# Kernel optimization log

Measured on AMD Instinct MI355X. Metric: run time of the kernel, lower is better.

## Reference

```python
import jax, jax.numpy as jnp
import numpy as np

N_EMBD = 1024
N_HEAD = 16
B, T = 2, 2048
LN_EPS = 1e-5


def _linear_params(key, d_in, d_out):
    k1, k2 = jax.random.split(key)
    bound = 1.0 / np.sqrt(d_in)
    W = jax.random.uniform(k1, (d_in, d_out), jnp.float32, -bound, bound)
    b = jax.random.uniform(k2, (d_out,), jnp.float32, -bound, bound)
    return W, b


def setup_inputs() -> dict:
    key = jax.random.key(0)
    ks = jax.random.split(key, 8)
    x = jax.random.normal(ks[0], (B, T, N_EMBD), jnp.float32)
    Wq, bq = _linear_params(ks[1], N_EMBD, N_EMBD)
    Wk, bk = _linear_params(ks[2], N_EMBD, N_EMBD)
    Wv, bv = _linear_params(ks[3], N_EMBD, N_EMBD)
    Wo, bo = _linear_params(ks[4], N_EMBD, N_EMBD)
    W1, b1 = _linear_params(ks[5], N_EMBD, 4 * N_EMBD)
    W2, b2 = _linear_params(ks[6], 4 * N_EMBD, N_EMBD)
    ln1_g = jnp.ones((N_EMBD,), jnp.float32)
    ln1_b = jnp.zeros((N_EMBD,), jnp.float32)
    ln2_g = jnp.ones((N_EMBD,), jnp.float32)
    ln2_b = jnp.zeros((N_EMBD,), jnp.float32)
    return dict(x=x, Wq=Wq, bq=bq, Wk=Wk, bk=bk, Wv=Wv, bv=bv, Wo=Wo, bo=bo,
                W1=W1, b1=b1, W2=W2, b2=b2,
                ln1_g=ln1_g, ln1_b=ln1_b, ln2_g=ln2_g, ln2_b=ln2_b)


def _layernorm(x, g, b):
    mu = jnp.mean(x, axis=-1, keepdims=True)
    var = jnp.mean(jnp.square(x - mu), axis=-1, keepdims=True)
    return (x - mu) * jax.lax.rsqrt(var + LN_EPS) * g + b


def _attention(x, Wq, bq, Wk, bk, Wv, bv, Wo, bo):
    Bsz, Tlen, C = x.shape
    hd = C // N_HEAD
    q = (x @ Wq + bq).reshape(Bsz, Tlen, N_HEAD, hd)
    k = (x @ Wk + bk).reshape(Bsz, Tlen, N_HEAD, hd)
    v = (x @ Wv + bv).reshape(Bsz, Tlen, N_HEAD, hd)
    scale = 1.0 / np.sqrt(hd)
    # NOTE: the original module's mask buffer is all ones -> masked_fill is a
    # no-op, so attention is FULL (non-causal) despite the class name.
    att = jnp.einsum('bqhd,bkhd->bhqk', q, k) * scale
    att = jax.nn.softmax(att, axis=-1)
    y = jnp.einsum('bhqk,bkhd->bqhd', att, v).reshape(Bsz, Tlen, C)
    return y @ Wo + bo


def reference(x, Wq, bq, Wk, bk, Wv, bv, Wo, bo, W1, b1, W2, b2,
              ln1_g, ln1_b, ln2_g, ln2_b):
    x = x + _attention(_layernorm(x, ln1_g, ln1_b), Wq, bq, Wk, bk, Wv, bv, Wo, bo)
    h = _layernorm(x, ln2_g, ln2_b)
    h = jax.nn.gelu(h @ W1 + b1, approximate=False) @ W2 + b2
    return x + h
```

## Files before the change

### kernel.cpp

```cpp
#include <hip/hip_runtime.h>
#include <hip/hip_bf16.h>
#include <math.h>


typedef __bf16 bf16x8 __attribute__((ext_vector_type(8)));
typedef float f32x4 __attribute__((ext_vector_type(4)));

__device__ __forceinline__ unsigned short f2bf(float f) {
  union { float f; unsigned int u; } v; v.f = f;
  unsigned int u = v.u;
  unsigned int r = (u + 0x7fffu + ((u >> 16) & 1u)) >> 16;
  return (unsigned short)r;
}

__device__ __forceinline__ unsigned int fbits(float f) {
  union { float f; unsigned int u; } v; v.f = f;
  return v.u;
}

__device__ __forceinline__ bf16x8 ld_bf16x8(const unsigned short* p) {
  union { uint4 u; bf16x8 v; } x;
  x.u = *(const uint4*)p;
  return x.v;
}

__device__ __forceinline__ float fast_exp2(float x) {
#if __has_builtin(__builtin_amdgcn_exp2f)
  return __builtin_amdgcn_exp2f(x);
#else
  return exp2f(x);
#endif
}

__device__ __forceinline__ void async_copy16(const void* g, void* l) {
  __builtin_amdgcn_global_load_lds(
      (const __attribute__((address_space(1))) void*)g,
      (__attribute__((address_space(3))) void*)l, 16, 0, 0);
}

__global__ __launch_bounds__(256) void transpose_cast_kernel(
    const float* __restrict__ W, unsigned short* __restrict__ Wt, int N, int K) {
  __shared__ unsigned short tile[32][33];
  const int n0 = blockIdx.x * 32, k0 = blockIdx.y * 32;
  const int t = threadIdx.x;
  const int r = t >> 3, cq = (t & 7) * 4;
  float4 v = *(const float4*)&W[(size_t)(k0 + r) * N + n0 + cq];
  tile[cq + 0][r] = f2bf(v.x);
  tile[cq + 1][r] = f2bf(v.y);
  tile[cq + 2][r] = f2bf(v.z);
  tile[cq + 3][r] = f2bf(v.w);
  __syncthreads();
  ushort4 o;
  o.x = tile[r][cq + 0];
  o.y = tile[r][cq + 1];
  o.z = tile[r][cq + 2];
  o.w = tile[r][cq + 3];
  *(ushort4*)&Wt[(size_t)(n0 + r) * K + k0 + cq] = o;
}

__global__ __launch_bounds__(256) void transpose_v_kernel(
    const unsigned short* __restrict__ V, unsigned short* __restrict__ Vt) {
  __shared__ unsigned short tile[32][36];
  const int kt = blockIdx.x * 32;
  const int d0 = blockIdx.y * 32;
  const int bh = blockIdx.z;
  const int bb = bh >> 4, h = bh & 15;
  const int t = threadIdx.x;
  const int r = t >> 3, c4 = (t & 7) * 4;
  ushort4 v = *(const ushort4*)&V[((size_t)bb * 2048 + kt + r) * 1024 + h * 64 + d0 + c4];
  tile[c4 + 0][r] = v.x;
  tile[c4 + 1][r] = v.y;
  tile[c4 + 2][r] = v.z;
  tile[c4 + 3][r] = v.w;
  __syncthreads();
  ushort4 o;
  o.x = tile[r][c4 + 0];
  o.y = tile[r][c4 + 1];
  o.z = tile[r][c4 + 2];
  o.w = tile[r][c4 + 3];
  *(ushort4*)&Vt[((size_t)bh * 64 + d0 + r) * 2048 + kt + c4] = o;
}

__global__ __launch_bounds__(256) void ln_kernel(
    const float* __restrict__ x, const float* __restrict__ g,
    const float* __restrict__ b, unsigned short* __restrict__ out) {
  const int row = blockIdx.x, t = threadIdx.x;
  const float4 v = ((const float4*)(x + (size_t)row * 1024))[t];
  float s = v.x + v.y + v.z + v.w;
  float s2 = v.x * v.x + v.y * v.y + v.z * v.z + v.w * v.w;
  for (int o = 32; o > 0; o >>= 1) {
    s += __shfl_xor(s, o, 64);
    s2 += __shfl_xor(s2, o, 64);
  }
  __shared__ float red[8];
  const int w = t >> 6;
  if ((t & 63) == 0) { red[w] = s; red[4 + w] = s2; }
  __syncthreads();
  s = red[0] + red[1] + red[2] + red[3];
  s2 = red[4] + red[5] + red[6] + red[7];
  const float mu = s * (1.f / 1024.f);
  const float var = s2 * (1.f / 1024.f) - mu * mu;
  const float rs = rsqrtf(var + 1e-5f);
  const float4 gg = ((const float4*)g)[t];
  const float4 bb = ((const float4*)b)[t];
  ushort4 o4;
  o4.x = f2bf((v.x - mu) * rs * gg.x + bb.x);
  o4.y = f2bf((v.y - mu) * rs * gg.y + bb.y);
  o4.z = f2bf((v.z - mu) * rs * gg.z + bb.z);
  o4.w = f2bf((v.w - mu) * rs * gg.w + bb.w);
  ((ushort4*)(out + (size_t)row * 1024))[t] = o4;
}

enum { MODE_QKV = 0, MODE_RES = 1, MODE_GELU = 2 };

#define QSCALE 0.18033688011112043f

template <int BM, int BN, int MODE>
__global__ __launch_bounds__(256) void gemm_kernel(
    const unsigned short* __restrict__ A, const unsigned short* __restrict__ Bt,
    const float* __restrict__ bias0, const float* __restrict__ bias1,
    const float* __restrict__ bias2, const float* __restrict__ residual,
    void* __restrict__ out0, void* __restrict__ out1, void* __restrict__ out2,
    int M, int N, int K) {
  constexpr int MI = BM / 32;
  constexpr int NI = BN / 32;
  __shared__ __align__(16) unsigned short As[2][2][BM * 32];
  __shared__ __align__(16) unsigned short Bs[2][2][BN * 32];
  const int t = threadIdx.x;

  const int NT = N / BN;
  const int NTX = NT >> 3;
  const int bid = blockIdx.x;
  const int xcd = bid & 7, local = bid >> 3;
  const int nt_ = xcd * NTX + local % NTX;
  const int mt = local / NTX;
  const int m0 = mt * BM, n0 = nt_ * BN;

  const int l = t & 63, w = t >> 6;
  const int wm = (w >> 1) * (BM / 2), wn = (w & 1) * (BN / 2);
  const int lr = l & 15, lq = l >> 4;

  f32x4 acc[MI][NI];
#pragma unroll
  for (int i = 0; i < MI; i++)
#pragma unroll
    for (int j = 0; j < NI; j++) {
      f32x4 z = {0.f, 0.f, 0.f, 0.f};
      acc[i][j] = z;
    }

  auto issue = [&](int k0, int p) {
#pragma unroll
    for (int h = 0; h < 2; h++)
#pragma unroll
      for (int s = 0; s < BM / 64; s++) {
        const int c = t + s * 256;
        const int row = c >> 2, k8 = (c & 3) * 8;
        async_copy16(&A[(size_t)(m0 + row) * K + k0 + h * 32 + k8],
                     &As[p][h][c * 8]);
      }
#pragma unroll
    for (int h = 0; h < 2; h++)
#pragma unroll
      for (int s = 0; s < BN / 64; s++) {
        const int c = t + s * 256;
        const int row = c >> 2, k8 = (c & 3) * 8;
        async_copy16(&Bt[(size_t)(n0 + row) * K + k0 + h * 32 + k8],
                     &Bs[p][h][c * 8]);
      }
  };

  issue(0, 0);
  int p = 0;
  for (int k0 = 0; k0 < K; k0 += 64) {
    __syncthreads();
    if (k0 + 64 < K) issue(k0 + 64, p ^ 1);
#pragma unroll
    for (int kk = 0; kk < 2; kk++) {
      bf16x8 af[MI], bf[NI];
#pragma unroll
      for (int mi = 0; mi < MI; mi++)
        af[mi] = ld_bf16x8(&As[p][kk][(wm + mi * 16 + lr) * 32 + lq * 8]);
#pragma unroll
      for (int ni = 0; ni < NI; ni++)
        bf[ni] = ld_bf16x8(&Bs[p][kk][(wn + ni * 16 + lr) * 32 + lq * 8]);
#pragma unroll
      for (int mi = 0; mi < MI; mi++)
#pragma unroll
        for (int ni = 0; ni < NI; ni++)
          acc[mi][ni] = __builtin_amdgcn_mfma_f32_16x16x32_bf16(
              af[mi], bf[ni], acc[mi][ni], 0, 0, 0);
    }
    p ^= 1;
  }

#pragma unroll
  for (int mi = 0; mi < MI; mi++) {
#pragma unroll
    for (int ni = 0; ni < NI; ni++) {
#pragma unroll
      for (int i = 0; i < 4; i++) {
        const int gm = m0 + wm + mi * 16 + lq * 4 + i;
        const int gn = n0 + wn + ni * 16 + lr;
        const float v = acc[mi][ni][i];
        if (MODE == MODE_QKV) {
          const int sel = gn >> 10, cn = gn & 1023;
          const float* bb = sel == 0 ? bias0 : (sel == 1 ? bias1 : bias2);
          unsigned short* dst =
              (unsigned short*)(sel == 0 ? out0 : (sel == 1 ? out1 : out2));
          float u = v + bb[cn];
          if (sel == 0) u *= QSCALE;
          dst[(size_t)gm * 1024 + cn] = f2bf(u);
        } else if (MODE == MODE_RES) {
          ((float*)out0)[(size_t)gm * N + gn] =
              v + bias0[gn] + residual[(size_t)gm * N + gn];
        } else {
          const float u = v + bias0[gn];
          const float ge = 0.5f * u * (1.f + erff(u * 0.70710678118654752f));
          ((unsigned short*)out0)[(size_t)gm * N + gn] = f2bf(ge);
        }
      }
    }
  }
}

__global__ __launch_bounds__(256) void attn_kernel(
    const unsigned short* __restrict__ Q, const unsigned short* __restrict__ Kt,
    const unsigned short* __restrict__ Vt, unsigned short* __restrict__ O) {
  __shared__ __align__(16) unsigned short Ps[128 * 72];
  const int id = blockIdx.x;
  const int xcd = id & 7, loc = id >> 3;
  const int bh = xcd * 4 + (loc >> 4);
  const int qt = loc & 15;
  const int bb = bh >> 4, h = bh & 15;
  const int t = threadIdx.x, l = t & 63, w = t >> 6;
  const int lr = l & 15, lq = l >> 4;
  const size_t rowBase = (size_t)bb * 2048;
  const int col0 = h * 64;

  bf16x8 qf[2][2];
#pragma unroll
  for (int s = 0; s < 2; s++)
#pragma unroll
    for (int kk = 0; kk < 2; kk++)
      qf[s][kk] = ld_bf16x8(
          &Q[(rowBase + qt * 128 + w * 32 + s * 16 + lr) * 1024 + col0 +
             kk * 32 + lq * 8]);

  bf16x8 kf[2][4];
#pragma unroll
  for (int nt = 0; nt < 4; nt++)
#pragma unroll
    for (int kk = 0; kk < 2; kk++)
      kf[kk][nt] = ld_bf16x8(
          &Kt[(rowBase + nt * 16 + lr) * 1024 + col0 + kk * 32 + lq * 8]);

  f32x4 oacc[2][4];
#pragma unroll
  for (int s = 0; s < 2; s++)
#pragma unroll
    for (int nt = 0; nt < 4; nt++) {
      f32x4 z = {0.f, 0.f, 0.f, 0.f};
      oacc[s][nt] = z;
    }
  float lp[2] = {0.f, 0.f};

  for (int kt = 0; kt < 2048; kt += 64) {
    bf16x8 vf[2][4];
#pragma unroll
    for (int nt = 0; nt < 4; nt++)
#pragma unroll
      for (int kb = 0; kb < 2; kb++)
        vf[kb][nt] = ld_bf16x8(
            &Vt[((size_t)bh * 64 + nt * 16 + lr) * 2048 + kt + kb * 32 +
                lq * 8]);

    f32x4 st[2][4];
#pragma unroll
    for (int s = 0; s < 2; s++)
#pragma unroll
      for (int nt = 0; nt < 4; nt++) {
        f32x4 z = {0.f, 0.f, 0.f, 0.f};
        st[s][nt] = z;
      }
#pragma unroll
    for (int nt = 0; nt < 4; nt++) {
      __builtin_amdgcn_s_setprio(1);
      st[0][nt] = __builtin_amdgcn_mfma_f32_16x16x32_bf16(kf[0][nt], qf[0][0], st[0][nt], 0, 0, 0);
      st[1][nt] = __builtin_amdgcn_mfma_f32_16x16x32_bf16(kf[0][nt], qf[1][0], st[1][nt], 0, 0, 0);
      st[0][nt] = __builtin_amdgcn_mfma_f32_16x16x32_bf16(kf[1][nt], qf[0][1], st[0][nt], 0, 0, 0);
      st[1][nt] = __builtin_amdgcn_mfma_f32_16x16x32_bf16(kf[1][nt], qf[1][1], st[1][nt], 0, 0, 0);
      __builtin_amdgcn_s_setprio(0);
    }

    const int ktn = (kt + 64) & 2047;
#pragma unroll
    for (int nt = 0; nt < 4; nt++)
#pragma unroll
      for (int kk = 0; kk < 2; kk++)
        kf[kk][nt] = ld_bf16x8(
            &Kt[(rowBase + ktn + nt * 16 + lr) * 1024 + col0 + kk * 32 +
                lq * 8]);

#pragma unroll
    for (int s = 0; s < 2; s++) {
      float rsum = 0.f;
#pragma unroll
      for (int nt = 0; nt < 4; nt++)
#pragma unroll
        for (int i = 0; i < 4; i++) {
          const float pv = fast_exp2(st[s][nt][i]);
          st[s][nt][i] = pv;
          rsum += pv;
        }
      lp[s] += rsum;
    }

#pragma unroll
    for (int s = 0; s < 2; s++)
#pragma unroll
      for (int nt = 0; nt < 4; nt++) {
        uint2 pk;
        pk.x = __builtin_amdgcn_perm(fbits(st[s][nt][1]), fbits(st[s][nt][0]), 0x07060302u);
        pk.y = __builtin_amdgcn_perm(fbits(st[s][nt][3]), fbits(st[s][nt][2]), 0x07060302u);
        *(uint2*)&Ps[(w * 32 + s * 16 + lr) * 72 + nt * 16 + lq * 4] = pk;
      }

#pragma unroll
    for (int kb = 0; kb < 2; kb++) {
      bf16x8 pf0 = ld_bf16x8(&Ps[(w * 32 + lr) * 72 + kb * 32 + lq * 8]);
      bf16x8 pf1 = ld_bf16x8(&Ps[(w * 32 + 16 + lr) * 72 + kb * 32 + lq * 8]);
      __builtin_amdgcn_s_setprio(1);
#pragma unroll
      for (int nt = 0; nt < 4; nt++) {
        oacc[0][nt] = __builtin_amdgcn_mfma_f32_16x16x32_bf16(pf0, vf[kb][nt], oacc[0][nt], 0, 0, 0);
        oacc[1][nt] = __builtin_amdgcn_mfma_f32_16x16x32_bf16(pf1, vf[kb][nt], oacc[1][nt], 0, 0, 0);
      }
      __builtin_amdgcn_s_setprio(0);
    }
  }

#pragma unroll
  for (int s = 0; s < 2; s++) {
    float li = lp[s];
    li += __shfl_xor(li, 16, 64);
    li += __shfl_xor(li, 32, 64);
    const float inv = 1.f / li;
#pragma unroll
    for (int nt = 0; nt < 4; nt++)
#pragma unroll
      for (int i = 0; i < 4; i++) {
        const size_t orow = rowBase + qt * 128 + w * 32 + s * 16 + lq * 4 + i;
        const int ocol = col0 + nt * 16 + lr;
        O[orow * 1024 + ocol] = f2bf(oacc[s][nt][i] * inv);
      }
  }
}

extern "C" void kernel_launch(void* const* d_in, const int* in_sizes, int n_in,
                              void* d_out, int out_size, void* d_ws, size_t ws_size,
                              hipStream_t stream) {
  const float* x    = (const float*)d_in[0];
  const float* Wq   = (const float*)d_in[1];
  const float* bq   = (const float*)d_in[2];
  const float* Wk   = (const float*)d_in[3];
  const float* bk   = (const float*)d_in[4];
  const float* Wv   = (const float*)d_in[5];
  const float* bv   = (const float*)d_in[6];
  const float* Wo   = (const float*)d_in[7];
  const float* bo   = (const float*)d_in[8];
  const float* W1   = (const float*)d_in[9];
  const float* b1   = (const float*)d_in[10];
  const float* W2   = (const float*)d_in[11];
  const float* b2   = (const float*)d_in[12];
  const float* ln1g = (const float*)d_in[13];
  const float* ln1b = (const float*)d_in[14];
  const float* ln2g = (const float*)d_in[15];
  const float* ln2b = (const float*)d_in[16];

  char* ws = (char*)d_ws;
  const size_t MB = 1024ull * 1024ull;
  unsigned short* WqT = (unsigned short*)(ws + 0 * MB);
  unsigned short* WkT = (unsigned short*)(ws + 2 * MB);
  unsigned short* WvT = (unsigned short*)(ws + 4 * MB);
  unsigned short* WoT = (unsigned short*)(ws + 6 * MB);
  unsigned short* W1T = (unsigned short*)(ws + 8 * MB);
  unsigned short* W2T = (unsigned short*)(ws + 16 * MB);
  unsigned short* xn  = (unsigned short*)(ws + 24 * MB);
  unsigned short* Qb  = (unsigned short*)(ws + 32 * MB);
  unsigned short* Kb  = (unsigned short*)(ws + 40 * MB);
  unsigned short* Vb  = (unsigned short*)(ws + 48 * MB);
  unsigned short* Ob  = (unsigned short*)(ws + 56 * MB);
  float*          x1  = (float*)(ws + 64 * MB);
  unsigned short* h2  = (unsigned short*)(ws + 80 * MB);
  unsigned short* VtG = (unsigned short*)(ws + 24 * MB);
  unsigned short* Hb  = (unsigned short*)(ws + 24 * MB);

  const dim3 blk(256);

  transpose_cast_kernel<<<dim3(32, 32), blk, 0, stream>>>(Wq, WqT, 1024, 1024);
  transpose_cast_kernel<<<dim3(32, 32), blk, 0, stream>>>(Wk, WkT, 1024, 1024);
  transpose_cast_kernel<<<dim3(32, 32), blk, 0, stream>>>(Wv, WvT, 1024, 1024);
  transpose_cast_kernel<<<dim3(32, 32), blk, 0, stream>>>(Wo, WoT, 1024, 1024);
  transpose_cast_kernel<<<dim3(128, 32), blk, 0, stream>>>(W1, W1T, 4096, 1024);
  transpose_cast_kernel<<<dim3(32, 128), blk, 0, stream>>>(W2, W2T, 1024, 4096);

  ln_kernel<<<4096, blk, 0, stream>>>(x, ln1g, ln1b, xn);

  gemm_kernel<128, 128, MODE_QKV><<<dim3(24 * 32), blk, 0, stream>>>(
      xn, WqT, bq, bk, bv, nullptr, Qb, Kb, Vb, 4096, 3072, 1024);

  transpose_v_kernel<<<dim3(64, 2, 32), blk, 0, stream>>>(Vb, VtG);

  attn_kernel<<<dim3(512), blk, 0, stream>>>(Qb, Kb, VtG, Ob);

  gemm_kernel<64, 128, MODE_RES><<<dim3(8 * 64), blk, 0, stream>>>(
      Ob, WoT, bo, nullptr, nullptr, x, x1, nullptr, nullptr, 4096, 1024, 1024);

  ln_kernel<<<4096, blk, 0, stream>>>(x1, ln2g, ln2b, h2);

  gemm_kernel<128, 128, MODE_GELU><<<dim3(32 * 32), blk, 0, stream>>>(
      h2, W1T, b1, nullptr, nullptr, nullptr, Hb, nullptr, nullptr, 4096, 4096, 1024);

  gemm_kernel<64, 128, MODE_RES><<<dim3(8 * 64), blk, 0, stream>>>(
      Hb, W2T, b2, nullptr, nullptr, x1, (float*)d_out, nullptr, nullptr, 4096, 1024, 4096);
}
```

Measured before the change: 448.2 us.

## Write Q/K/V from QKV GEMM in MFMA-fragment-packed layout, drop V transpose

The QKV GEMM epilogue now scatters Q, K and V directly into a packed layout matching the attention kernel's per-lane MFMA fragment order, including V pre-transposed. This removes the separate V transpose kernel and makes the attention kernel's fragment loads contiguous 1 KB chunks per wavefront instead of strided rows. The cost is scattered 2-byte stores in the GEMM epilogue, which may coalesce worse.

Measured after the change: 372.2 us. 16.9% less time.

```diff
diff --git a/kernel.cpp b/kernel.cpp
--- a/kernel.cpp
+++ b/kernel.cpp
@@ -56,29 +56,6 @@
   o.z = tile[r][cq + 2];
   o.w = tile[r][cq + 3];
   *(ushort4*)&Wt[(size_t)(n0 + r) * K + k0 + cq] = o;
-}
-
-__global__ __launch_bounds__(256) void transpose_v_kernel(
-    const unsigned short* __restrict__ V, unsigned short* __restrict__ Vt) {
-  __shared__ unsigned short tile[32][36];
-  const int kt = blockIdx.x * 32;
-  const int d0 = blockIdx.y * 32;
-  const int bh = blockIdx.z;
-  const int bb = bh >> 4, h = bh & 15;
-  const int t = threadIdx.x;
-  const int r = t >> 3, c4 = (t & 7) * 4;
-  ushort4 v = *(const ushort4*)&V[((size_t)bb * 2048 + kt + r) * 1024 + h * 64 + d0 + c4];
-  tile[c4 + 0][r] = v.x;
-  tile[c4 + 1][r] = v.y;
-  tile[c4 + 2][r] = v.z;
-  tile[c4 + 3][r] = v.w;
-  __syncthreads();
-  ushort4 o;
-  o.x = tile[r][c4 + 0];
-  o.y = tile[r][c4 + 1];
-  o.z = tile[r][c4 + 2];
-  o.w = tile[r][c4 + 3];
-  *(ushort4*)&Vt[((size_t)bh * 64 + d0 + r) * 2048 + kt + c4] = o;
 }
 
 __global__ __launch_bounds__(256) void ln_kernel(
@@ -205,12 +182,36 @@
         const float v = acc[mi][ni][i];
         if (MODE == MODE_QKV) {
           const int sel = gn >> 10, cn = gn & 1023;
-          const float* bb = sel == 0 ? bias0 : (sel == 1 ? bias1 : bias2);
-          unsigned short* dst =
-              (unsigned short*)(sel == 0 ? out0 : (sel == 1 ? out1 : out2));
-          float u = v + bb[cn];
-          if (sel == 0) u *= QSCALE;
-          dst[(size_t)gm * 1024 + cn] = f2bf(u);
+          const int hh = cn >> 6, d = cn & 63;
+          const int bb2 = gm >> 11, tok = gm & 2047;
+          const size_t bh = (size_t)bb2 * 16 + hh;
+          float u = v + (sel == 0 ? bias0 : (sel == 1 ? bias1 : bias2))[cn];
+          if (sel == 0) {
+            u *= QSCALE;
+            const int qt = tok >> 7, r7 = tok & 127;
+            const int ww = r7 >> 5, ss = (r7 >> 4) & 1, qlr = r7 & 15;
+            const int kk = d >> 5, lq2 = (d >> 3) & 3, e = d & 7;
+            const size_t idx =
+                (((((bh * 16 + qt) * 4 + ww) * 2 + ss) * 2 + kk) << 9) +
+                (lq2 * 16 + qlr) * 8 + e;
+            ((unsigned short*)out0)[idx] = f2bf(u);
+          } else if (sel == 1) {
+            const int ktile = tok >> 6, r6 = tok & 63;
+            const int nt2 = r6 >> 4, klr = r6 & 15;
+            const int kk = d >> 5, lq2 = (d >> 3) & 3, e = d & 7;
+            const size_t idx =
+                ((((bh * 32 + ktile) * 4 + nt2) * 2 + kk) << 9) +
+                (lq2 * 16 + klr) * 8 + e;
+            ((unsigned short*)out1)[idx] = f2bf(u);
+          } else {
+            const int ktile = tok >> 6, r6 = tok & 63;
+            const int kb = r6 >> 5, lq2 = (r6 >> 3) & 3, e = r6 & 7;
+            const int nt2 = d >> 4, vlr = d & 15;
+            const size_t idx =
+                ((((bh * 32 + ktile) * 2 + kb) * 4 + nt2) << 9) +
+                (lq2 * 16 + vlr) * 8 + e;
+            ((unsigned short*)out2)[idx] = f2bf(u);
+          }
         } else if (MODE == MODE_RES) {
           ((float*)out0)[(size_t)gm * N + gn] =
               v + bias0[gn] + residual[(size_t)gm * N + gn];
@@ -225,35 +226,36 @@
 }
 
 __global__ __launch_bounds__(256) void attn_kernel(
-    const unsigned short* __restrict__ Q, const unsigned short* __restrict__ Kt,
-    const unsigned short* __restrict__ Vt, unsigned short* __restrict__ O) {
+    const unsigned short* __restrict__ Qp, const unsigned short* __restrict__ Kp,
+    const unsigned short* __restrict__ Vp, unsigned short* __restrict__ O) {
   __shared__ __align__(16) unsigned short Ps[128 * 72];
   const int id = blockIdx.x;
   const int xcd = id & 7, loc = id >> 3;
   const int bh = xcd * 4 + (loc >> 4);
   const int qt = loc & 15;
-  const int bb = bh >> 4, h = bh & 15;
   const int t = threadIdx.x, l = t & 63, w = t >> 6;
   const int lr = l & 15, lq = l >> 4;
-  const size_t rowBase = (size_t)bb * 2048;
-  const int col0 = h * 64;
-
+  const int l8 = l * 8;
+  const size_t rowBase = (size_t)(bh >> 4) * 2048;
+  const int col0 = (bh & 15) * 64;
+
+  const unsigned short* Qb_ = Qp + ((((size_t)bh * 16 + qt) * 4 + w) << 11);
   bf16x8 qf[2][2];
 #pragma unroll
   for (int s = 0; s < 2; s++)
 #pragma unroll
     for (int kk = 0; kk < 2; kk++)
-      qf[s][kk] = ld_bf16x8(
-          &Q[(rowBase + qt * 128 + w * 32 + s * 16 + lr) * 1024 + col0 +
-             kk * 32 + lq * 8]);
+      qf[s][kk] = ld_bf16x8(&Qb_[((s * 2 + kk) << 9) + l8]);
+
+  const unsigned short* Kb_ = Kp + ((size_t)bh << 17);
+  const unsigned short* Vb_ = Vp + ((size_t)bh << 17);
 
   bf16x8 kf[2][4];
 #pragma unroll
   for (int nt = 0; nt < 4; nt++)
 #pragma unroll
     for (int kk = 0; kk < 2; kk++)
-      kf[kk][nt] = ld_bf16x8(
-          &Kt[(rowBase + nt * 16 + lr) * 1024 + col0 + kk * 32 + lq * 8]);
+      kf[kk][nt] = ld_bf16x8(&Kb_[((nt * 2 + kk) << 9) + l8]);
 
   f32x4 oacc[2][4];
 #pragma unroll
@@ -265,15 +267,14 @@
     }
   float lp[2] = {0.f, 0.f};
 
-  for (int kt = 0; kt < 2048; kt += 64) {
+  for (int kt = 0; kt < 32; kt++) {
+    const unsigned short* vtile = Vb_ + ((size_t)kt << 12);
     bf16x8 vf[2][4];
 #pragma unroll
-    for (int nt = 0; nt < 4; nt++)
-#pragma unroll
-      for (int kb = 0; kb < 2; kb++)
-        vf[kb][nt] = ld_bf16x8(
-            &Vt[((size_t)bh * 64 + nt * 16 + lr) * 2048 + kt + kb * 32 +
-                lq * 8]);
+    for (int kb = 0; kb < 2; kb++)
+#pragma unroll
+      for (int nt = 0; nt < 4; nt++)
+        vf[kb][nt] = ld_bf16x8(&vtile[((kb * 4 + nt) << 9) + l8]);
 
     f32x4 st[2][4];
 #pragma unroll
@@ -293,14 +294,12 @@
       __builtin_amdgcn_s_setprio(0);
     }
 
-    const int ktn = (kt + 64) & 2047;
+    const unsigned short* ktile_p = Kb_ + ((size_t)((kt + 1) & 31) << 12);
 #pragma unroll
     for (int nt = 0; nt < 4; nt++)
 #pragma unroll
       for (int kk = 0; kk < 2; kk++)
-        kf[kk][nt] = ld_bf16x8(
-            &Kt[(rowBase + ktn + nt * 16 + lr) * 1024 + col0 + kk * 32 +
-                lq * 8]);
+        kf[kk][nt] = ld_bf16x8(&ktile_p[((nt * 2 + kk) << 9) + l8]);
 
 #pragma unroll
     for (int s = 0; s < 2; s++) {
@@ -387,13 +386,12 @@
   unsigned short* W1T = (unsigned short*)(ws + 8 * MB);
   unsigned short* W2T = (unsigned short*)(ws + 16 * MB);
   unsigned short* xn  = (unsigned short*)(ws + 24 * MB);
-  unsigned short* Qb  = (unsigned short*)(ws + 32 * MB);
-  unsigned short* Kb  = (unsigned short*)(ws + 40 * MB);
-  unsigned short* Vb  = (unsigned short*)(ws + 48 * MB);
+  unsigned short* Qp  = (unsigned short*)(ws + 32 * MB);
+  unsigned short* Kp  = (unsigned short*)(ws + 40 * MB);
+  unsigned short* Vp  = (unsigned short*)(ws + 48 * MB);
   unsigned short* Ob  = (unsigned short*)(ws + 56 * MB);
   float*          x1  = (float*)(ws + 64 * MB);
   unsigned short* h2  = (unsigned short*)(ws + 80 * MB);
-  unsigned short* VtG = (unsigned short*)(ws + 24 * MB);
   unsigned short* Hb  = (unsigned short*)(ws + 24 * MB);
 
   const dim3 blk(256);
@@ -408,11 +406,9 @@
   ln_kernel<<<4096, blk, 0, stream>>>(x, ln1g, ln1b, xn);
 
   gemm_kernel<128, 128, MODE_QKV><<<dim3(24 * 32), blk, 0, stream>>>(
-      xn, WqT, bq, bk, bv, nullptr, Qb, Kb, Vb, 4096, 3072, 1024);
-
-  transpose_v_kernel<<<dim3(64, 2, 32), blk, 0, stream>>>(Vb, VtG);
-
-  attn_kernel<<<dim3(512), blk, 0, stream>>>(Qb, Kb, VtG, Ob);
+      xn, WqT, bq, bk, bv, nullptr, Qp, Kp, Vp, 4096, 3072, 1024);
+
+  attn_kernel<<<dim3(512), blk, 0, stream>>>(Qp, Kp, Vp, Ob);
 
   gemm_kernel<64, 128, MODE_RES><<<dim3(8 * 64), blk, 0, stream>>>(
       Ob, WoT, bo, nullptr, nullptr, x, x1, nullptr, nullptr, 4096, 1024, 1024);
```
